# Kernel tuning notes

Hardware: AMD Instinct MI355X
Metric: run time of the kernel (lower is better)

## Reference

```python
import jax, jax.numpy as jnp
import numpy as np

N_NODES = 50000
N_EDGES = 800000
NUM_GRAPHS = 512
EMB = 128
OUT_DIM = 2145 * 2
EPS_BN = 1e-5
EPS_GN = 1e-5


def gat_conv(x, src, dst, W, att_s, att_d, bias, n):
    # PyG GATConv, heads=1: h = x W ; alpha_e = leakyrelu(a_s.h[src] + a_d.h[dst])
    h = x @ W                                   # [N, EMB]
    a_s = h @ att_s                             # [N]
    a_d = h @ att_d                             # [N]
    logits = jax.nn.leaky_relu(a_s[src] + a_d[dst], 0.2)   # [E]
    m = jax.ops.segment_max(logits, dst, num_segments=n)
    ex = jnp.exp(logits - m[dst])
    denom = jax.ops.segment_sum(ex, dst, num_segments=n)
    alpha = ex / (denom[dst] + 1e-16)           # segment softmax over in-edges
    out = jax.ops.segment_sum(alpha[:, None] * h[src], dst, num_segments=n)
    return out + bias


def setup_inputs() -> dict:
    key = jax.random.key(0)
    ks = jax.random.split(key, 16)
    x = jax.random.normal(ks[0], (N_NODES, 1), dtype=jnp.float32)
    edge_index = jax.random.randint(ks[1], (2, N_EDGES), 0, N_NODES, dtype=jnp.int64)
    batch = jnp.sort(jax.random.randint(ks[2], (N_NODES,), 0, NUM_GRAPHS, dtype=jnp.int64))
    edge_attr = jax.random.normal(ks[3], (N_EDGES, 1), dtype=jnp.float32)
    s = 0.1
    return {
        "x": x, "edge_index": edge_index, "batch": batch, "edge_attr": edge_attr,
        "W0": jax.random.normal(ks[4], (1, EMB), dtype=jnp.float32) * s,
        "as0": jax.random.normal(ks[5], (EMB,), dtype=jnp.float32) * s,
        "ad0": jax.random.normal(ks[6], (EMB,), dtype=jnp.float32) * s,
        "b0": jnp.zeros((EMB,), dtype=jnp.float32),
        "W1": jax.random.normal(ks[7], (EMB, EMB), dtype=jnp.float32) * s,
        "as1": jax.random.normal(ks[8], (EMB,), dtype=jnp.float32) * s,
        "ad1": jax.random.normal(ks[9], (EMB,), dtype=jnp.float32) * s,
        "b1": jnp.zeros((EMB,), dtype=jnp.float32),
        "bn_g": jnp.ones((EMB,), dtype=jnp.float32),
        "bn_b": jnp.zeros((EMB,), dtype=jnp.float32),
        "gn_w": jnp.ones((EMB,), dtype=jnp.float32),
        "gn_b": jnp.zeros((EMB,), dtype=jnp.float32),
        "gn_ms": jnp.ones((EMB,), dtype=jnp.float32),
        "Wout": jax.random.normal(ks[10], (2 * EMB, OUT_DIM), dtype=jnp.float32) * s,
        "bout": jnp.zeros((OUT_DIM,), dtype=jnp.float32),
    }


def reference(x, edge_index, batch, edge_attr, W0, as0, ad0, b0, W1, as1, ad1, b1,
              bn_g, bn_b, gn_w, gn_b, gn_ms, Wout, bout):
    n = x.shape[0]
    # PyG GATConv add_self_loops=True
    loops = jnp.arange(n, dtype=edge_index.dtype)
    src = jnp.concatenate([edge_index[0], loops])
    dst = jnp.concatenate([edge_index[1], loops])
    # edge_attr ignored (edge_dim=None in GATConv)

    h = jnp.tanh(gat_conv(x, src, dst, W0, as0, ad0, b0, n))
    # dropout p=0.2 treated as identity (deterministic eval reference)

    # BatchNorm over nodes (training/batch statistics)
    mu = jnp.mean(h, axis=0)
    var = jnp.mean((h - mu) ** 2, axis=0)
    h = bn_g * (h - mu) / jnp.sqrt(var + EPS_BN) + bn_b

    # GraphNorm: per-graph mean-scale normalization
    cnt = jax.ops.segment_sum(jnp.ones((n,), h.dtype), batch, num_segments=NUM_GRAPHS)[:, None]
    gmean = jax.ops.segment_sum(h, batch, num_segments=NUM_GRAPHS) / cnt
    h0 = h - gmean[batch] * gn_ms
    gvar = jax.ops.segment_sum(h0 ** 2, batch, num_segments=NUM_GRAPHS) / cnt
    h = gn_w * h0 / jnp.sqrt(gvar[batch] + EPS_GN) + gn_b

    h = jnp.tanh(gat_conv(h, src, dst, W1, as1, ad1, b1, n))

    # global max + mean pool per graph
    pmax = jax.ops.segment_max(h, batch, num_segments=NUM_GRAPHS)
    pmean = jax.ops.segment_sum(h, batch, num_segments=NUM_GRAPHS) / cnt
    pooled = jnp.concatenate([pmax, pmean], axis=1)   # [G, 2*EMB]
    return pooled @ Wout + bout                        # [G, OUT_DIM]
```

## Files before the change

### kernel.cpp

```cpp
#include <hip/hip_runtime.h>
#include <hip/hip_fp16.h>
#include <math.h>

#define EMB 128
#define NGRAPH 512
#define MAXBUCK 800
#define BCAP 1536
#define CHUNK 8192

typedef _Float16 f16_t;
typedef _Float16 f16x8 __attribute__((ext_vector_type(8)));
typedef float f32x4 __attribute__((ext_vector_type(4)));

__device__ __forceinline__ float leaky(float v){ return v > 0.f ? v : 0.2f*v; }
__device__ __forceinline__ float ftanh(float x){
    float u = __expf(2.f*x);
    return 1.f - 2.f*__builtin_amdgcn_rcpf(u + 1.f);
}
__device__ __forceinline__ float frcp(float x){ return __builtin_amdgcn_rcpf(x); }

__global__ __launch_bounds__(256) void k_misc(const float* W0, const float* as0, const float* ad0,
                                              float* c_sd, const float* W1, f16_t* W1t,
                                              const float* Wout, int OUT, f16_t* WoutT){
    __shared__ f16_t lt[64*68];
    __shared__ float s1[128], s2[128];
    int b = blockIdx.x;
    int t = threadIdx.x;
    if(b < 272){
        int n0 = (b%68)*64, k0 = (b/68)*64;
        #pragma unroll
        for(int j=0;j<16;j++){
            int k_l = (t>>6)*16 + j;
            int n_l = t&63;
            int n = n0+n_l;
            float v = (n < OUT) ? Wout[(size_t)(k0+k_l)*OUT + n] : 0.f;
            lt[n_l*68 + k_l] = (f16_t)v;
        }
        __syncthreads();
        #pragma unroll
        for(int j=0;j<16;j++){
            int n_l = (t>>6)*16 + j;
            int k_l = t&63;
            WoutT[(size_t)(n0+n_l)*256 + k0 + k_l] = lt[n_l*68 + k_l];
        }
    } else if(b < 336){
        int idx = (b-272)*256 + t;
        int n = idx>>7, k = idx&127;
        W1t[n*128+k] = (f16_t)W1[k*128+n];
    } else {
        if(t<128){ float w = W0[t]; s1[t]=w*as0[t]; s2[t]=w*ad0[t]; }
        __syncthreads();
        for(int off=64; off>0; off>>=1){
            if(t<off){ s1[t]+=s1[t+off]; s2[t]+=s2[t+off]; }
            __syncthreads();
        }
        if(t==0){ c_sd[0]=s1[0]; c_sd[1]=s2[0]; }
    }
}

__global__ void k_bcount(const int* dst, int E, int nbuck, int* bcnt){
    __shared__ int h[MAXBUCK];
    int t = threadIdx.x;
    for(int j=t;j<MAXBUCK;j+=512) h[j]=0;
    __syncthreads();
    int stride = gridDim.x*blockDim.x;
    for(int e = blockIdx.x*blockDim.x+t; e<E; e+=stride)
        atomicAdd(&h[dst[e]>>6], 1);
    __syncthreads();
    for(int j=t;j<nbuck;j+=512) if(h[j]) atomicAdd(&bcnt[j], h[j]);
}

__global__ void k_bscan(const int* bcnt, int nbuck, int* bbase, int* bcursor){
    __shared__ int s[1024];
    int t = threadIdx.x;
    int own = (t<nbuck)? bcnt[t] : 0;
    s[t] = own;
    __syncthreads();
    for(int off=1; off<1024; off<<=1){
        int a = (t>=off)? s[t-off] : 0;
        __syncthreads();
        s[t] += a;
        __syncthreads();
    }
    if(t<nbuck){ int ex = s[t]-own; bbase[t]=ex; bcursor[t]=ex; }
    if(t==nbuck-1) bbase[nbuck]=s[t];
}

__global__ void k_gseg(const int* batch, int N, int* gstart){
    int i = blockIdx.x*blockDim.x+threadIdx.x;
    if(i>=N) return;
    int b = batch[i];
    if(i==0){ for(int g=0;g<=b;g++) gstart[g]=0; }
    else { int bp=batch[i-1]; for(int g=bp+1; g<=b; g++) gstart[g]=i; }
    if(i==N-1){ for(int g=b+1; g<=NGRAPH; g++) gstart[g]=N; }
}

__global__ __launch_bounds__(512) void k_bscatter(const int* src, const int* dst, int E,
                                                  int nbuck, int* bcursor, unsigned* ebuf){
    __shared__ int cnt[MAXBUCK];
    __shared__ int loff[MAXBUCK];
    __shared__ int cur[MAXBUCK];
    __shared__ int gbase[MAXBUCK];
    __shared__ int s[1024];
    __shared__ unsigned srt[CHUNK];
    int t = threadIdx.x;
    int c0 = blockIdx.x*CHUNK;
    int m = E - c0; if(m > CHUNK) m = CHUNK;
    for(int j=t;j<MAXBUCK;j+=512) cnt[j]=0;
    __syncthreads();
    unsigned rec[16];
    #pragma unroll
    for(int u=0;u<16;u++){
        int j = u*512 + t;
        if(j<m){
            int d = dst[c0+j];
            int sv = src[c0+j];
            rec[u] = ((unsigned)(d>>6)<<22) | ((unsigned)(d&63)<<16) | (unsigned)sv;
            atomicAdd(&cnt[d>>6], 1);
        } else rec[u] = 0xFFFFFFFFu;
    }
    __syncthreads();
    int v0 = (t<nbuck)? cnt[t]:0;
    int j2 = t+512;
    int v1 = (j2<nbuck)? cnt[j2]:0;
    s[t]=v0; s[j2]=v1;
    __syncthreads();
    for(int off=1; off<1024; off<<=1){
        int a = (t>=off)? s[t-off]:0;
        int b = s[j2-off];
        __syncthreads();
        s[t]+=a; s[j2]+=b;
        __syncthreads();
    }
    for(int j=t;j<nbuck;j+=512){
        int c = cnt[j];
        int ex = s[j]-c;
        loff[j]=ex; cur[j]=ex;
        if(c>0) gbase[j]=atomicAdd(&bcursor[j], c);
    }
    __syncthreads();
    #pragma unroll
    for(int u=0;u<16;u++){
        if(rec[u]!=0xFFFFFFFFu){
            int b = rec[u]>>22;
            int p = atomicAdd(&cur[b],1);
            srt[p]=rec[u];
        }
    }
    __syncthreads();
    for(int j=t;j<m;j+=512){
        unsigned r = srt[j];
        int b = r>>22;
        ebuf[gbase[b] + (j - loff[b])] = r;
    }
}

__global__ __launch_bounds__(256) void k_gat0(const unsigned* ebuf, const int* bbase,
                                              const float* x, const float* c_sd,
                                              int N, float* s0,
                                              unsigned short* csr16, int* rowstart){
    __shared__ unsigned raw[BCAP];
    __shared__ unsigned short esrc[BCAP];
    __shared__ int cnt[64], off[64], cur[64];
    int t = threadIdx.x;
    int b = blockIdx.x;
    int e0 = bbase[b];
    int m = bbase[b+1]-e0; if(m>BCAP) m=BCAP;
    for(int j=t;j<m;j+=256) raw[j]=ebuf[e0+j];
    if(t<64) cnt[t]=0;
    __syncthreads();
    for(int j=t;j<m;j+=256) atomicAdd(&cnt[(raw[j]>>16)&63],1);
    __syncthreads();
    if(t<64){
        int v = cnt[t]; int inc = v;
        #pragma unroll
        for(int o=1;o<64;o<<=1){ int u = __shfl_up(inc,o); if(t>=o) inc+=u; }
        off[t]=inc-v; cur[t]=inc-v;
    }
    __syncthreads();
    for(int j=t;j<m;j+=256){
        unsigned r=raw[j]; int n=(r>>16)&63;
        int p=atomicAdd(&cur[n],1);
        esrc[p]=(unsigned short)(r&0xFFFF);
    }
    __syncthreads();
    for(int j=t;j<m;j+=256) csr16[e0+j]=esrc[j];
    if(t<64) rowstart[b*64+t] = e0 + off[t];
    int n = t>>2, sub = t&3;
    int gid = b*64 + n;
    if(gid>=N) return;
    float cs=c_sd[0], cd=c_sd[1];
    float xi = x[gid]; float adi = cd*xi;
    int r0=off[n], r1=cur[n];
    float den=0.f, num=0.f;
    if(sub==0){
        float ex = __expf(leaky(fmaf(cs,xi,adi)));
        den=ex; num=ex*xi;
    }
    for(int e=r0+sub;e<r1;e+=4){
        float xs = x[esrc[e]];
        float ee = __expf(leaky(fmaf(cs,xs,adi)));
        den += ee; num = fmaf(ee,xs,num);
    }
    den += __shfl_xor(den,1); den += __shfl_xor(den,2);
    num += __shfl_xor(num,1); num += __shfl_xor(num,2);
    if(sub==0) s0[gid] = num*frcp(den+1e-16f);
}

__global__ void k_gstats(const float* s0, const int* gstart, const float* W0, const float* b0,
                         float* gsum, float* gsumsq){
    int g=blockIdx.x, k=threadIdx.x;
    float wk=W0[k], bk=b0[k];
    int i0=gstart[g], i1=gstart[g+1];
    float s=0.f, q=0.f;
    for(int i=i0;i<i1;i++){
        float t=ftanh(fmaf(s0[i],wk,bk));
        s+=t; q=fmaf(t,t,q);
    }
    gsum[g*EMB+k]=s; gsumsq[g*EMB+k]=q;
}

__global__ void k_bnstats(const float* gsum, const float* gsumsq,
                          const float* bn_g, const float* bn_b, int N,
                          float* bnsc, float* bnsh){
    int k=threadIdx.x;
    float cs=0.f, cq=0.f;
    for(int g=0; g<NGRAPH; g++){ cs+=gsum[g*EMB+k]; cq+=gsumsq[g*EMB+k]; }
    float invN = 1.f/(float)N;
    float mu=cs*invN; float var = cq*invN - mu*mu;
    float sc = bn_g[k]*rsqrtf(var+1e-5f);
    bnsc[k]=sc; bnsh[k]=bn_b[k]-mu*sc;
}

__global__ void k_pq(const float* gsum, const float* gsumsq, const int* gstart,
                     const float* bnsc, const float* bnsh,
                     const float* gn_w, const float* gn_b, const float* gn_ms,
                     float* P, float* Q){
    int idx = blockIdx.x*blockDim.x+threadIdx.x;
    int g = idx>>7, k = idx&127;
    int c = gstart[g+1]-gstart[g];
    float rc = frcp((float)(c>0?c:1));
    float m1 = gsum[idx]*rc, m2 = gsumsq[idx]*rc;
    float A = bnsc[k], Bs = bnsh[k];
    float gmean = fmaf(A,m1,Bs);
    float B = Bs - gmean*gn_ms[k];
    float gvar = A*A*m2 + 2.f*A*B*m1 + B*B;
    float rg = rsqrtf(gvar+1e-5f);
    float w = gn_w[k];
    P[idx] = w*A*rg;
    Q[idx] = fmaf(w*B, rg, gn_b[k]);
}

__global__ void k_H(const float* s0, const int* batch, const float* W0, const float* b0,
                    const float* P, const float* Q, int N, f16_t* H){
    int total = N*16;
    int stride = gridDim.x*blockDim.x;
    for(int idx = blockIdx.x*blockDim.x+threadIdx.x; idx < total; idx += stride){
        int i = idx>>4;
        int k0 = (idx&15)*8;
        float s = s0[i]; int g = batch[i];
        const float* Pg=&P[g*EMB+k0]; const float* Qg=&Q[g*EMB+k0];
        const float* W0p=&W0[k0]; const float* b0p=&b0[k0];
        f16x8 o;
        #pragma unroll
        for(int u=0;u<8;u++){
            o[u] = (f16_t)fmaf(Pg[u], ftanh(fmaf(s,W0p[u],b0p[u])), Qg[u]);
        }
        *(f16x8*)&H[(size_t)i*EMB + k0] = o;
    }
}

__global__ __launch_bounds__(256) void k_gemm1(const f16_t* H, const f16_t* W1t,
        const float* as1, const float* ad1,
        int N, f16_t* h1, float* a_s, float* a_d){
    __shared__ f16_t ob[64*136];
    int t = threadIdx.x;
    int i0 = blockIdx.x*64;
    int w = t>>6, l = t&63;
    int lm = l&15, lq = l>>4;
    int arow = i0 + w*16 + lm; if(arow > N-1) arow = N-1;
    const f16_t* ap = &H[(size_t)arow*EMB + lq*8];
    f16x8 a[4];
    #pragma unroll
    for(int kt=0;kt<4;kt++) a[kt] = *(const f16x8*)&ap[kt*32];
    f32x4 acc[8];
    #pragma unroll
    for(int nt=0;nt<8;nt++) acc[nt] = (f32x4){0.f,0.f,0.f,0.f};
    #pragma unroll
    for(int nt=0;nt<8;nt++){
        const f16_t* bp = &W1t[(nt*16 + lm)*128 + lq*8];
        f16x8 b0v = *(const f16x8*)&bp[0];
        f16x8 b1v = *(const f16x8*)&bp[32];
        f16x8 b2v = *(const f16x8*)&bp[64];
        f16x8 b3v = *(const f16x8*)&bp[96];
        acc[nt] = __builtin_amdgcn_mfma_f32_16x16x32_f16(a[0], b0v, acc[nt], 0, 0, 0);
        acc[nt] = __builtin_amdgcn_mfma_f32_16x16x32_f16(a[1], b1v, acc[nt], 0, 0, 0);
        acc[nt] = __builtin_amdgcn_mfma_f32_16x16x32_f16(a[2], b2v, acc[nt], 0, 0, 0);
        acc[nt] = __builtin_amdgcn_mfma_f32_16x16x32_f16(a[3], b3v, acc[nt], 0, 0, 0);
    }
    float ps[4] = {0.f,0.f,0.f,0.f};
    float pd[4] = {0.f,0.f,0.f,0.f};
    #pragma unroll
    for(int nt=0;nt<8;nt++){
        int n = nt*16 + lm;
        float asv = as1[n], adv = ad1[n];
        #pragma unroll
        for(int r=0;r<4;r++){
            ps[r] = fmaf(acc[nt][r], asv, ps[r]);
            pd[r] = fmaf(acc[nt][r], adv, pd[r]);
        }
    }
    #pragma unroll
    for(int r=0;r<4;r++){
        #pragma unroll
        for(int off=1; off<16; off<<=1){
            ps[r] += __shfl_xor(ps[r], off);
            pd[r] += __shfl_xor(pd[r], off);
        }
    }
    if(lm==0){
        #pragma unroll
        for(int r=0;r<4;r++){
            int i = i0 + w*16 + lq*4 + r;
            if(i < N){ a_s[i]=ps[r]; a_d[i]=pd[r]; }
        }
    }
    #pragma unroll
    for(int nt=0;nt<8;nt++){
        int n = nt*16 + lm;
        #pragma unroll
        for(int r=0;r<4;r++){
            int row = w*16 + lq*4 + r;
            ob[row*136 + n] = (f16_t)acc[nt][r];
        }
    }
    __syncthreads();
    #pragma unroll
    for(int c=0;c<4;c++){
        int idx = t + 256*c;
        int row = idx>>4, q = idx&15;
        int i = i0 + row;
        if(i < N){
            f16x8 v = *(const f16x8*)&ob[row*136 + q*8];
            *(f16x8*)&h1[(size_t)i*EMB + q*8] = v;
        }
    }
}

__global__ __launch_bounds__(256) void k_gat1(const unsigned short* csr16, const int* rowstart,
                                              const f16_t* h1, const float* a_s, const float* a_d,
                                              const float* b1, int N, f16_t* h2){
    int wave = threadIdx.x>>6, lane = threadIdx.x&63;
    int i = blockIdx.x*4 + wave;
    if(i>=N) return;
    int r0=rowstart[i], r1=rowstart[i+1]; int deg=r1-r0;
    float adi = a_d[i];
    float exs = __expf(leaky(a_s[i] + adi) - 4.f);
    const __half2* h1v = (const __half2*)h1;
    float2 hv = __half22float2(h1v[(size_t)i*64 + lane]);
    float2 acc0; acc0.x = exs*hv.x; acc0.y = exs*hv.y;
    float2 acc1 = {0.f,0.f}, acc2 = {0.f,0.f}, acc3 = {0.f,0.f};
    float denp = (lane==0)? exs : 0.f;
    for(int c=0;c<deg;c+=64){
        int e = c+lane;
        unsigned pk = 0;
        if(e<deg){
            int s = (int)csr16[r0+e];
            float ex = __expf(leaky(a_s[s]+adi)-4.f);
            denp += ex;
            pk = (unsigned)s | ((unsigned)__half_as_ushort(__float2half(ex))<<16);
        }
        int cnt = min(64, deg-c);
        int jj=0;
        for(; jj+7<cnt; jj+=8){
            unsigned p0=__shfl(pk,jj+0), p1=__shfl(pk,jj+1), p2=__shfl(pk,jj+2), p3=__shfl(pk,jj+3);
            unsigned p4=__shfl(pk,jj+4), p5=__shfl(pk,jj+5), p6=__shfl(pk,jj+6), p7=__shfl(pk,jj+7);
            float2 v0 = __half22float2(h1v[(size_t)(p0&0xFFFF)*64 + lane]);
            float2 v1 = __half22float2(h1v[(size_t)(p1&0xFFFF)*64 + lane]);
            float2 v2 = __half22float2(h1v[(size_t)(p2&0xFFFF)*64 + lane]);
            float2 v3 = __half22float2(h1v[(size_t)(p3&0xFFFF)*64 + lane]);
            float2 v4 = __half22float2(h1v[(size_t)(p4&0xFFFF)*64 + lane]);
            float2 v5 = __half22float2(h1v[(size_t)(p5&0xFFFF)*64 + lane]);
            float2 v6 = __half22float2(h1v[(size_t)(p6&0xFFFF)*64 + lane]);
            float2 v7 = __half22float2(h1v[(size_t)(p7&0xFFFF)*64 + lane]);
            float a0=__half2float(__ushort_as_half((unsigned short)(p0>>16)));
            float a1=__half2float(__ushort_as_half((unsigned short)(p1>>16)));
            float a2=__half2float(__ushort_as_half((unsigned short)(p2>>16)));
            float a3=__half2float(__ushort_as_half((unsigned short)(p3>>16)));
            float a4=__half2float(__ushort_as_half((unsigned short)(p4>>16)));
            float a5=__half2float(__ushort_as_half((unsigned short)(p5>>16)));
            float a6=__half2float(__ushort_as_half((unsigned short)(p6>>16)));
            float a7=__half2float(__ushort_as_half((unsigned short)(p7>>16)));
            acc0.x = fmaf(a0, v0.x, acc0.x); acc0.y = fmaf(a0, v0.y, acc0.y);
            acc1.x = fmaf(a1, v1.x, acc1.x); acc1.y = fmaf(a1, v1.y, acc1.y);
            acc2.x = fmaf(a2, v2.x, acc2.x); acc2.y = fmaf(a2, v2.y, acc2.y);
            acc3.x = fmaf(a3, v3.x, acc3.x); acc3.y = fmaf(a3, v3.y, acc3.y);
            acc0.x = fmaf(a4, v4.x, acc0.x); acc0.y = fmaf(a4, v4.y, acc0.y);
            acc1.x = fmaf(a5, v5.x, acc1.x); acc1.y = fmaf(a5, v5.y, acc1.y);
            acc2.x = fmaf(a6, v6.x, acc2.x); acc2.y = fmaf(a6, v6.y, acc2.y);
            acc3.x = fmaf(a7, v7.x, acc3.x); acc3.y = fmaf(a7, v7.y, acc3.y);
        }
        for(; jj<cnt; jj++){
            unsigned p0=__shfl(pk,jj);
            float2 v0 = __half22float2(h1v[(size_t)(p0&0xFFFF)*64 + lane]);
            float a0=__half2float(__ushort_as_half((unsigned short)(p0>>16)));
            acc0.x = fmaf(a0, v0.x, acc0.x); acc0.y = fmaf(a0, v0.y, acc0.y);
        }
    }
    acc0.x += acc1.x + acc2.x + acc3.x;
    acc0.y += acc1.y + acc2.y + acc3.y;
    for(int o=32; o; o>>=1) denp += __shfl_xor(denp, o);
    float rden = frcp(denp + 1e-16f);
    float2 bb = *(const float2*)&b1[lane*2];
    float ox = ftanh(fmaf(acc0.x, rden, bb.x));
    float oy = ftanh(fmaf(acc0.y, rden, bb.y));
    *(__half2*)&h2[(size_t)i*EMB + lane*2] = __floats2half2_rn(ox, oy);
}

__global__ void k_pool(const f16_t* h2, const int* gstart, f16_t* pooled){
    int g=blockIdx.x, k=threadIdx.x;
    const __half2* h2v = (const __half2*)h2;
    int i0=gstart[g], i1=gstart[g+1];
    float2 mx = {-1e30f,-1e30f}, sm = {0.f,0.f};
    for(int i=i0;i<i1;i++){
        float2 v=__half22float2(h2v[(size_t)i*64+k]);
        mx.x=fmaxf(mx.x,v.x); mx.y=fmaxf(mx.y,v.y);
        sm.x+=v.x; sm.y+=v.y;
    }
    float c = frcp((float)((i1-i0)>0 ? (i1-i0) : 1));
    pooled[g*256+2*k  ]=(f16_t)mx.x;
    pooled[g*256+2*k+1]=(f16_t)mx.y;
    pooled[g*256+128+2*k  ]=(f16_t)(sm.x*c);
    pooled[g*256+128+2*k+1]=(f16_t)(sm.y*c);
}

__global__ __launch_bounds__(256) void k_out(const f16_t* pooled, const f16_t* WoutT,
                                             const float* bout, int OUT, float* out){
    int t = threadIdx.x;
    int w = t>>6, l = t&63;
    int lm = l&15, lq = l>>4;
    int m0 = (blockIdx.y*4 + w)*16;
    int n0 = blockIdx.x*64;
    f16x8 a[8];
    const f16_t* ap = &pooled[(m0+lm)*256 + lq*8];
    #pragma unroll
    for(int kt=0;kt<8;kt++) a[kt] = *(const f16x8*)&ap[kt*32];
    f32x4 acc[4];
    #pragma unroll
    for(int nt=0;nt<4;nt++) acc[nt] = (f32x4){0.f,0.f,0.f,0.f};
    #pragma unroll
    for(int nt=0;nt<4;nt++){
        const f16_t* bp = &WoutT[(size_t)(n0 + nt*16 + lm)*256 + lq*8];
        #pragma unroll
        for(int kt=0;kt<8;kt++){
            f16x8 b = *(const f16x8*)&bp[kt*32];
            acc[nt] = __builtin_amdgcn_mfma_f32_16x16x32_f16(a[kt], b, acc[nt], 0, 0, 0);
        }
    }
    #pragma unroll
    for(int nt=0;nt<4;nt++){
        int n = n0 + nt*16 + lm;
        if(n >= OUT) continue;
        float bv = bout[n];
        #pragma unroll
        for(int r=0;r<4;r++){
            int m = m0 + lq*4 + r;
            out[(size_t)m*OUT + n] = acc[nt][r] + bv;
        }
    }
}

extern "C" void kernel_launch(void* const* d_in, const int* in_sizes, int n_in,
                              void* d_out, int out_size, void* d_ws, size_t ws_size,
                              hipStream_t stream) {
    const float* x    = (const float*)d_in[0];
    const int*   eidx = (const int*)d_in[1];
    const int*   batch= (const int*)d_in[2];
    const float* W0   = (const float*)d_in[4];
    const float* as0  = (const float*)d_in[5];
    const float* ad0  = (const float*)d_in[6];
    const float* b0   = (const float*)d_in[7];
    const float* W1   = (const float*)d_in[8];
    const float* as1  = (const float*)d_in[9];
    const float* ad1  = (const float*)d_in[10];
    const float* b1   = (const float*)d_in[11];
    const float* bn_g = (const float*)d_in[12];
    const float* bn_b = (const float*)d_in[13];
    const float* gn_w = (const float*)d_in[14];
    const float* gn_b = (const float*)d_in[15];
    const float* gn_ms= (const float*)d_in[16];
    const float* Wout = (const float*)d_in[17];
    const float* bout = (const float*)d_in[18];

    int N = in_sizes[0];
    int E = in_sizes[1]/2;
    int OUT = out_size / NGRAPH;
    const int* srcp = eidx;
    const int* dstp = eidx + E;
    int nbuck = (N+63)>>6;

    char* w = (char*)d_ws;
    auto alloc = [&](size_t bytes) -> void* {
        void* p = (void*)w; w += (bytes+255)&~(size_t)255; return p;
    };
    int* bcnt     = (int*)alloc(MAXBUCK*4);
    int* bbase    = (int*)alloc((MAXBUCK+1)*4);
    int* bcursor  = (int*)alloc(MAXBUCK*4);
    unsigned* ebuf= (unsigned*)alloc((size_t)E*4);
    unsigned short* csr16 = (unsigned short*)alloc((size_t)E*2);
    int* rowstart = (int*)alloc((size_t)(MAXBUCK*64+64)*4);
    float* c_sd   = (float*)alloc(256);
    float* s0     = (float*)alloc((size_t)N*4);
    int* gstart   = (int*)alloc((NGRAPH+1)*4);
    float* gsum   = (float*)alloc(NGRAPH*EMB*4);
    float* gsq    = (float*)alloc(NGRAPH*EMB*4);
    float* bnsc   = (float*)alloc(512);
    float* bnsh   = (float*)alloc(512);
    float* P      = (float*)alloc(NGRAPH*EMB*4);
    float* Q      = (float*)alloc(NGRAPH*EMB*4);
    f16_t* Hbuf   = (f16_t*)alloc((size_t)N*EMB*2);
    f16_t* h1     = (f16_t*)alloc((size_t)N*EMB*2);
    f16_t* h2     = (f16_t*)alloc((size_t)N*EMB*2);
    float* a_sv   = (float*)alloc((size_t)N*4);
    float* a_dv   = (float*)alloc((size_t)N*4);
    f16_t* pooled = (f16_t*)alloc(NGRAPH*256*2);
    f16_t* w1t    = (f16_t*)alloc(128*128*2);
    f16_t* woutt  = (f16_t*)alloc((size_t)4352*256*2);

    hipMemsetAsync(bcnt, 0, MAXBUCK*4, stream);

    k_misc<<<337,256,0,stream>>>(W0,as0,ad0,c_sd,W1,w1t,Wout,OUT,woutt);
    k_bcount<<<120,512,0,stream>>>(dstp,E,nbuck,bcnt);
    k_bscan<<<1,1024,0,stream>>>(bcnt,nbuck,bbase,bcursor);
    int nchunk = (E+CHUNK-1)/CHUNK;
    k_bscatter<<<nchunk,512,0,stream>>>(srcp,dstp,E,nbuck,bcursor,ebuf);
    k_gseg<<<(N+255)/256,256,0,stream>>>(batch,N,gstart);
    k_gat0<<<nbuck,256,0,stream>>>(ebuf,bbase,x,c_sd,N,s0,csr16,rowstart);
    k_gstats<<<NGRAPH,128,0,stream>>>(s0,gstart,W0,b0,gsum,gsq);
    k_bnstats<<<1,128,0,stream>>>(gsum,gsq,bn_g,bn_b,N,bnsc,bnsh);
    k_pq<<<(NGRAPH*EMB)/256,256,0,stream>>>(gsum,gsq,gstart,bnsc,bnsh,gn_w,gn_b,gn_ms,P,Q);
    k_H<<<1024,256,0,stream>>>(s0,batch,W0,b0,P,Q,N,Hbuf);
    k_gemm1<<<(N+63)/64,256,0,stream>>>(Hbuf,w1t,as1,ad1,N,h1,a_sv,a_dv);
    k_gat1<<<(N+3)/4,256,0,stream>>>(csr16,rowstart,h1,a_sv,a_dv,b1,N,h2);
    k_pool<<<NGRAPH,64,0,stream>>>(h2,gstart,pooled);
    dim3 og(68, 8);
    k_out<<<og,256,0,stream>>>(pooled,woutt,bout,OUT,(float*)d_out);
}
```

Before: 191.6 us.

## Fuse bucket count and graph segmentation into misc kernel, fold stats into gat0

Merges the bucket-count and graph-start kernels into the prologue misc kernel as extra block ranges. It also folds per-graph and per-column statistics into the layer-0 attention kernel using shared-memory segmented sums plus global atomics, and moves the BatchNorm finalisation into k_pq. This removes four launches along with the serial per-graph stats kernel and the single-block BN kernel. In exchange it adds float atomics, which make summation order nondeterministic, and it zeroes a larger buffer with one memset.

```diff
diff --git a/kernel.cpp b/kernel.cpp
--- a/kernel.cpp
+++ b/kernel.cpp
@@ -21,9 +21,12 @@
 
 __global__ __launch_bounds__(256) void k_misc(const float* W0, const float* as0, const float* ad0,
                                               float* c_sd, const float* W1, f16_t* W1t,
-                                              const float* Wout, int OUT, f16_t* WoutT){
+                                              const float* Wout, int OUT, f16_t* WoutT,
+                                              const int* dst, int E, int nbuck, int* bcnt,
+                                              const int* batch, int N, int* gstart){
     __shared__ f16_t lt[64*68];
     __shared__ float s1[128], s2[128];
+    __shared__ int h[MAXBUCK];
     int b = blockIdx.x;
     int t = threadIdx.x;
     if(b < 272){
@@ -47,7 +50,7 @@
         int idx = (b-272)*256 + t;
         int n = idx>>7, k = idx&127;
         W1t[n*128+k] = (f16_t)W1[k*128+n];
-    } else {
+    } else if(b == 336){
         if(t<128){ float w = W0[t]; s1[t]=w*as0[t]; s2[t]=w*ad0[t]; }
         __syncthreads();
         for(int off=64; off>0; off>>=1){
@@ -55,19 +58,23 @@
             __syncthreads();
         }
         if(t==0){ c_sd[0]=s1[0]; c_sd[1]=s2[0]; }
-    }
-}
-
-__global__ void k_bcount(const int* dst, int E, int nbuck, int* bcnt){
-    __shared__ int h[MAXBUCK];
-    int t = threadIdx.x;
-    for(int j=t;j<MAXBUCK;j+=512) h[j]=0;
-    __syncthreads();
-    int stride = gridDim.x*blockDim.x;
-    for(int e = blockIdx.x*blockDim.x+t; e<E; e+=stride)
-        atomicAdd(&h[dst[e]>>6], 1);
-    __syncthreads();
-    for(int j=t;j<nbuck;j+=512) if(h[j]) atomicAdd(&bcnt[j], h[j]);
+    } else if(b < 457){
+        int bb = b-337;
+        for(int j=t;j<MAXBUCK;j+=256) h[j]=0;
+        __syncthreads();
+        int stride = 120*256;
+        for(int e = bb*256+t; e<E; e+=stride)
+            atomicAdd(&h[dst[e]>>6], 1);
+        __syncthreads();
+        for(int j=t;j<nbuck;j+=256) if(h[j]) atomicAdd(&bcnt[j], h[j]);
+    } else {
+        int i = (b-457)*256 + t;
+        if(i>=N) return;
+        int b2 = batch[i];
+        if(i==0){ for(int g=0;g<=b2;g++) gstart[g]=0; }
+        else { int bp=batch[i-1]; for(int g=bp+1; g<=b2; g++) gstart[g]=i; }
+        if(i==N-1){ for(int g=b2+1; g<=NGRAPH; g++) gstart[g]=N; }
+    }
 }
 
 __global__ void k_bscan(const int* bcnt, int nbuck, int* bbase, int* bcursor){
@@ -84,15 +91,6 @@
     }
     if(t<nbuck){ int ex = s[t]-own; bbase[t]=ex; bcursor[t]=ex; }
     if(t==nbuck-1) bbase[nbuck]=s[t];
-}
-
-__global__ void k_gseg(const int* batch, int N, int* gstart){
-    int i = blockIdx.x*blockDim.x+threadIdx.x;
-    if(i>=N) return;
-    int b = batch[i];
-    if(i==0){ for(int g=0;g<=b;g++) gstart[g]=0; }
-    else { int bp=batch[i-1]; for(int g=bp+1; g<=b; g++) gstart[g]=i; }
-    if(i==N-1){ for(int g=b+1; g<=NGRAPH; g++) gstart[g]=N; }
 }
 
 __global__ __launch_bounds__(512) void k_bscatter(const int* src, const int* dst, int E,
@@ -157,11 +155,17 @@
 
 __global__ __launch_bounds__(256) void k_gat0(const unsigned* ebuf, const int* bbase,
                                               const float* x, const float* c_sd,
+                                              const int* batch, const float* W0, const float* b0,
                                               int N, float* s0,
-                                              unsigned short* csr16, int* rowstart){
+                                              unsigned short* csr16, int* rowstart,
+                                              float* gsum, float* gsq,
+                                              float* colsum, float* colsq){
     __shared__ unsigned raw[BCAP];
     __shared__ unsigned short esrc[BCAP];
     __shared__ int cnt[64], off[64], cur[64];
+    __shared__ float s0l[64];
+    __shared__ int bl[64];
+    __shared__ float totl[256], totql[256];
     int t = threadIdx.x;
     int b = blockIdx.x;
     int e0 = bbase[b];
@@ -185,63 +189,79 @@
     }
     __syncthreads();
     for(int j=t;j<m;j+=256) csr16[e0+j]=esrc[j];
-    if(t<64) rowstart[b*64+t] = e0 + off[t];
-    int n = t>>2, sub = t&3;
-    int gid = b*64 + n;
-    if(gid>=N) return;
-    float cs=c_sd[0], cd=c_sd[1];
-    float xi = x[gid]; float adi = cd*xi;
-    int r0=off[n], r1=cur[n];
-    float den=0.f, num=0.f;
-    if(sub==0){
-        float ex = __expf(leaky(fmaf(cs,xi,adi)));
-        den=ex; num=ex*xi;
-    }
-    for(int e=r0+sub;e<r1;e+=4){
-        float xs = x[esrc[e]];
-        float ee = __expf(leaky(fmaf(cs,xs,adi)));
-        den += ee; num = fmaf(ee,xs,num);
-    }
-    den += __shfl_xor(den,1); den += __shfl_xor(den,2);
-    num += __shfl_xor(num,1); num += __shfl_xor(num,2);
-    if(sub==0) s0[gid] = num*frcp(den+1e-16f);
-}
-
-__global__ void k_gstats(const float* s0, const int* gstart, const float* W0, const float* b0,
-                         float* gsum, float* gsumsq){
-    int g=blockIdx.x, k=threadIdx.x;
-    float wk=W0[k], bk=b0[k];
-    int i0=gstart[g], i1=gstart[g+1];
-    float s=0.f, q=0.f;
-    for(int i=i0;i<i1;i++){
-        float t=ftanh(fmaf(s0[i],wk,bk));
-        s+=t; q=fmaf(t,t,q);
-    }
-    gsum[g*EMB+k]=s; gsumsq[g*EMB+k]=q;
-}
-
-__global__ void k_bnstats(const float* gsum, const float* gsumsq,
-                          const float* bn_g, const float* bn_b, int N,
-                          float* bnsc, float* bnsh){
-    int k=threadIdx.x;
-    float cs=0.f, cq=0.f;
-    for(int g=0; g<NGRAPH; g++){ cs+=gsum[g*EMB+k]; cq+=gsumsq[g*EMB+k]; }
-    float invN = 1.f/(float)N;
-    float mu=cs*invN; float var = cq*invN - mu*mu;
-    float sc = bn_g[k]*rsqrtf(var+1e-5f);
-    bnsc[k]=sc; bnsh[k]=bn_b[k]-mu*sc;
-}
-
-__global__ void k_pq(const float* gsum, const float* gsumsq, const int* gstart,
-                     const float* bnsc, const float* bnsh,
+    if(t<64){
+        rowstart[b*64+t] = e0 + off[t];
+        int gid2 = b*64+t;
+        bl[t] = (gid2<N) ? batch[gid2] : -1;
+    }
+    {
+        int n = t>>2, sub = t&3;
+        int gid = b*64 + n;
+        if(gid < N){
+            float cs=c_sd[0], cd=c_sd[1];
+            float xi = x[gid]; float adi = cd*xi;
+            int r0=off[n], r1=cur[n];
+            float den=0.f, num=0.f;
+            if(sub==0){
+                float ex = __expf(leaky(fmaf(cs,xi,adi)));
+                den=ex; num=ex*xi;
+            }
+            for(int e=r0+sub;e<r1;e+=4){
+                float xs = x[esrc[e]];
+                float ee = __expf(leaky(fmaf(cs,xs,adi)));
+                den += ee; num = fmaf(ee,xs,num);
+            }
+            den += __shfl_xor(den,1); den += __shfl_xor(den,2);
+            num += __shfl_xor(num,1); num += __shfl_xor(num,2);
+            if(sub==0){ float v = num*frcp(den+1e-16f); s0[gid]=v; s0l[n]=v; }
+        }
+    }
+    __syncthreads();
+    {
+        int k = t&127, half = t>>7;
+        float wk = W0[k], bk = b0[k];
+        int base = half*32;
+        float sum=0.f, sq=0.f, tot=0.f, totq=0.f;
+        int curg = -1;
+        #pragma unroll 4
+        for(int u=0;u<32;u++){
+            int n = base+u;
+            int g2 = bl[n];
+            if(g2 < 0) break;
+            float tv = ftanh(fmaf(s0l[n],wk,bk));
+            if(g2!=curg){
+                if(curg>=0){ atomicAdd(&gsum[curg*EMB+k],sum); atomicAdd(&gsq[curg*EMB+k],sq); }
+                curg=g2; sum=0.f; sq=0.f;
+            }
+            sum+=tv; sq=fmaf(tv,tv,sq);
+            tot+=tv; totq=fmaf(tv,tv,totq);
+        }
+        if(curg>=0){ atomicAdd(&gsum[curg*EMB+k],sum); atomicAdd(&gsq[curg*EMB+k],sq); }
+        totl[t]=tot; totql[t]=totq;
+    }
+    __syncthreads();
+    if(t<128){
+        float a = totl[t]+totl[t+128];
+        float q = totql[t]+totql[t+128];
+        if(a!=0.f || q!=0.f){ atomicAdd(&colsum[t],a); atomicAdd(&colsq[t],q); }
+    }
+}
+
+__global__ void k_pq(const float* gsum, const float* gsq, const int* gstart,
+                     const float* colsum, const float* colsq,
+                     const float* bn_g, const float* bn_b,
                      const float* gn_w, const float* gn_b, const float* gn_ms,
-                     float* P, float* Q){
+                     int N, float* P, float* Q){
     int idx = blockIdx.x*blockDim.x+threadIdx.x;
     int g = idx>>7, k = idx&127;
+    float invN = frcp((float)N);
+    float mu = colsum[k]*invN;
+    float var = colsq[k]*invN - mu*mu;
+    float A = bn_g[k]*rsqrtf(var+1e-5f);
+    float Bs = bn_b[k]-mu*A;
     int c = gstart[g+1]-gstart[g];
     float rc = frcp((float)(c>0?c:1));
-    float m1 = gsum[idx]*rc, m2 = gsumsq[idx]*rc;
-    float A = bnsc[k], Bs = bnsh[k];
+    float m1 = gsum[idx]*rc, m2 = gsq[idx]*rc;
     float gmean = fmaf(A,m1,Bs);
     float B = Bs - gmean*gn_ms[k];
     float gvar = A*A*m2 + 2.f*A*B*m1 + B*B;
@@ -503,7 +523,13 @@
     auto alloc = [&](size_t bytes) -> void* {
         void* p = (void*)w; w += (bytes+255)&~(size_t)255; return p;
     };
-    int* bcnt     = (int*)alloc(MAXBUCK*4);
+    size_t zbytes = (size_t)MAXBUCK*4 + 256*4 + 2*(size_t)NGRAPH*EMB*4;
+    char* zbuf    = (char*)alloc(zbytes);
+    int* bcnt     = (int*)zbuf;
+    float* colsum = (float*)(zbuf + MAXBUCK*4);
+    float* colsq  = colsum + 128;
+    float* gsum   = (float*)(zbuf + MAXBUCK*4 + 256*4);
+    float* gsq    = gsum + (size_t)NGRAPH*EMB;
     int* bbase    = (int*)alloc((MAXBUCK+1)*4);
     int* bcursor  = (int*)alloc(MAXBUCK*4);
     unsigned* ebuf= (unsigned*)alloc((size_t)E*4);
@@ -512,10 +538,6 @@
     float* c_sd   = (float*)alloc(256);
     float* s0     = (float*)alloc((size_t)N*4);
     int* gstart   = (int*)alloc((NGRAPH+1)*4);
-    float* gsum   = (float*)alloc(NGRAPH*EMB*4);
-    float* gsq    = (float*)alloc(NGRAPH*EMB*4);
-    float* bnsc   = (float*)alloc(512);
-    float* bnsh   = (float*)alloc(512);
     float* P      = (float*)alloc(NGRAPH*EMB*4);
     float* Q      = (float*)alloc(NGRAPH*EMB*4);
     f16_t* Hbuf   = (f16_t*)alloc((size_t)N*EMB*2);
@@ -527,18 +549,18 @@
     f16_t* w1t    = (f16_t*)alloc(128*128*2);
     f16_t* woutt  = (f16_t*)alloc((size_t)4352*256*2);
 
-    hipMemsetAsync(bcnt, 0, MAXBUCK*4, stream);
-
-    k_misc<<<337,256,0,stream>>>(W0,as0,ad0,c_sd,W1,w1t,Wout,OUT,woutt);
-    k_bcount<<<120,512,0,stream>>>(dstp,E,nbuck,bcnt);
+    hipMemsetAsync(zbuf, 0, zbytes, stream);
+
+    int miscgrid = 457 + (N+255)/256;
+    k_misc<<<miscgrid,256,0,stream>>>(W0,as0,ad0,c_sd,W1,w1t,Wout,OUT,woutt,
+                                      dstp,E,nbuck,bcnt,batch,N,gstart);
     k_bscan<<<1,1024,0,stream>>>(bcnt,nbuck,bbase,bcursor);
     int nchunk = (E+CHUNK-1)/CHUNK;
     k_bscatter<<<nchunk,512,0,stream>>>(srcp,dstp,E,nbuck,bcursor,ebuf);
-    k_gseg<<<(N+255)/256,256,0,stream>>>(batch,N,gstart);
-    k_gat0<<<nbuck,256,0,stream>>>(ebuf,bbase,x,c_sd,N,s0,csr16,rowstart);
-    k_gstats<<<NGRAPH,128,0,stream>>>(s0,gstart,W0,b0,gsum,gsq);
-    k_bnstats<<<1,128,0,stream>>>(gsum,gsq,bn_g,bn_b,N,bnsc,bnsh);
-    k_pq<<<(NGRAPH*EMB)/256,256,0,stream>>>(gsum,gsq,gstart,bnsc,bnsh,gn_w,gn_b,gn_ms,P,Q);
+    k_gat0<<<nbuck,256,0,stream>>>(ebuf,bbase,x,c_sd,batch,W0,b0,N,s0,csr16,rowstart,
+                                   gsum,gsq,colsum,colsq);
+    k_pq<<<(NGRAPH*EMB)/256,256,0,stream>>>(gsum,gsq,gstart,colsum,colsq,
+                                            bn_g,bn_b,gn_w,gn_b,gn_ms,N,P,Q);
     k_H<<<1024,256,0,stream>>>(s0,batch,W0,b0,P,Q,N,Hbuf);
     k_gemm1<<<(N+63)/64,256,0,stream>>>(Hbuf,w1t,as1,ad1,N,h1,a_sv,a_dv);
     k_gat1<<<(N+3)/4,256,0,stream>>>(csr16,rowstart,h1,a_sv,a_dv,b1,N,h2);
```

Result: faster. 184.9 us (-3.5%).
